# Kernel tuning notes

Measured on AMD Instinct MI355X. Metric: run time of the kernel, lower is better.

Reference implementation:

```python
import jax, jax.numpy as jnp
import numpy as np

N_NODES = 50000
N_EDGES = 800000
N_GRAPHS = 512
F_IN = 128
H = 64


def setup_inputs() -> dict:
    key = jax.random.key(0)
    ks = jax.random.split(key, 12)
    x = jax.random.normal(ks[0], (N_NODES, F_IN), dtype=jnp.float32)
    edge_index = jax.random.randint(ks[1], (2, N_EDGES), 0, N_NODES, dtype=jnp.int64)
    batch = jnp.sort(jax.random.randint(ks[2], (N_NODES,), 0, N_GRAPHS, dtype=jnp.int64))
    def glorot(k, shape):
        lim = float(np.sqrt(6.0 / (shape[0] + shape[1])))
        return jax.random.uniform(k, shape, jnp.float32, -lim, lim)
    return {
        "x": x,
        "edge_index": edge_index,
        "batch": batch,
        "W1": glorot(ks[3], (F_IN, H)), "b1": jnp.zeros((H,), jnp.float32),
        "W2": glorot(ks[4], (H, H)),    "b2": jnp.zeros((H,), jnp.float32),
        "Wf1": glorot(ks[5], (H, 128)), "bf1": jnp.zeros((128,), jnp.float32),
        "Wf2": glorot(ks[6], (128, 1)), "bf2": jnp.zeros((1,), jnp.float32),
    }


def gcn_conv(x, src, dst, norm, W, b):
    # x' = D^{-1/2}(A+I)D^{-1/2} (x W) + b   (self-loops already in src/dst)
    xw = x @ W                                   # [N, H]
    msgs = xw[src] * norm[:, None]               # gather + scale, [E+N, H]
    agg = jax.ops.segment_sum(msgs, dst, num_segments=N_NODES)  # scatter-add
    return agg + b


def reference(x, edge_index, batch, W1, b1, W2, b2, Wf1, bf1, Wf2, bf2):
    loops = jnp.arange(N_NODES, dtype=edge_index.dtype)
    src = jnp.concatenate([edge_index[0], loops])
    dst = jnp.concatenate([edge_index[1], loops])
    # symmetric normalization: deg computed with self-loops, counted at dst
    deg = jax.ops.segment_sum(jnp.ones_like(dst, dtype=x.dtype), dst, num_segments=N_NODES)
    dinv = jax.lax.rsqrt(jnp.maximum(deg, 1.0))
    norm = dinv[src] * dinv[dst]

    h = jax.nn.relu(gcn_conv(x, src, dst, norm, W1, b1))
    h = jax.nn.relu(gcn_conv(h, src, dst, norm, W2, b2))

    # global mean pool over graphs
    sums = jax.ops.segment_sum(h, batch, num_segments=N_GRAPHS)      # [G, H]
    cnts = jax.ops.segment_sum(jnp.ones((N_NODES,), h.dtype), batch, num_segments=N_GRAPHS)
    pooled = sums / jnp.maximum(cnts, 1.0)[:, None]

    out = jax.nn.relu(pooled @ Wf1 + bf1)
    out = out @ Wf2 + bf2
    return out.squeeze(-1)
```

## Files before the change

kernel.cpp:

```cpp
#include <hip/hip_runtime.h>
#include <hip/hip_fp16.h>

#define N_NODES 50000
#define N_EDGES 800000
#define N_GRAPHS 512
#define F_IN 128
#define HDIM 64
#define NBUCK 196
#define BCAP 5120
#define EPB 4096
#define N_P1 ((N_EDGES + EPB - 1) / EPB)
#define MAXPER 20

__global__ __launch_bounds__(256) void pass1_k(const int* __restrict__ src, const int* __restrict__ dst,
                                               int* __restrict__ bucketTot, int* __restrict__ stage) {
    __shared__ int cnt[256];
    __shared__ int goff[256];
    int t = threadIdx.x;
    cnt[t] = 0;
    __syncthreads();
    int base = blockIdx.x * EPB + t * 16;
    int packed[16], meta[16];
    bool full = (blockIdx.x + 1) * EPB <= N_EDGES;
    if (full) {
        const int4* s4 = (const int4*)(src + base);
        const int4* d4 = (const int4*)(dst + base);
        #pragma unroll
        for (int q = 0; q < 4; ++q) {
            int4 sv = s4[q], dv = d4[q];
            int ss[4] = {sv.x, sv.y, sv.z, sv.w};
            int dd[4] = {dv.x, dv.y, dv.z, dv.w};
            #pragma unroll
            for (int j = 0; j < 4; ++j) {
                int b = dd[j] >> 8;
                int r = atomicAdd(&cnt[b], 1);
                packed[q * 4 + j] = ss[j] | ((dd[j] & 255) << 16);
                meta[q * 4 + j] = r | (b << 16);
            }
        }
    } else {
        #pragma unroll
        for (int k = 0; k < 16; ++k) {
            int e = base + k;
            if (e < N_EDGES) {
                int d = dst[e];
                int b = d >> 8;
                int r = atomicAdd(&cnt[b], 1);
                packed[k] = src[e] | ((d & 255) << 16);
                meta[k] = r | (b << 16);
            } else meta[k] = -1;
        }
    }
    __syncthreads();
    if (cnt[t] > 0) goff[t] = atomicAdd(&bucketTot[t], cnt[t]);
    __syncthreads();
    #pragma unroll
    for (int k = 0; k < 16; ++k) {
        if (meta[k] >= 0) {
            int b = meta[k] >> 16, r = meta[k] & 0xFFFF;
            stage[b * BCAP + goff[b] + r] = packed[k];
        }
    }
}

__global__ __launch_bounds__(256) void scanB_k(const int* __restrict__ bucketTot, int* __restrict__ bucketBase,
                                               int* __restrict__ row) {
    __shared__ int s[256];
    int t = threadIdx.x;
    int v = (t < NBUCK) ? bucketTot[t] : 0;
    s[t] = v; __syncthreads();
    for (int off = 1; off < 256; off <<= 1) {
        int u = (t >= off) ? s[t - off] : 0; __syncthreads();
        s[t] += u; __syncthreads();
    }
    if (t < NBUCK) bucketBase[t] = s[t] - v;
    if (t == 0) row[N_NODES] = N_EDGES;
}

__global__ __launch_bounds__(256) void pass2_k(const int* __restrict__ stage, const int* __restrict__ bucketTot,
                                               const int* __restrict__ bucketBase, int* __restrict__ row,
                                               float* __restrict__ dinv, int* __restrict__ csr) {
    __shared__ int cnt[256];
    __shared__ int pf[256];
    __shared__ int lcsr[BCAP];
    int b = blockIdx.x, t = threadIdx.x;
    int tot = bucketTot[b], base = bucketBase[b];
    cnt[t] = 0; __syncthreads();
    int myp[MAXPER], myr[MAXPER];
    #pragma unroll
    for (int k = 0; k < MAXPER; ++k) {
        int i = t + k * 256;
        if (i < tot) {
            int p = stage[b * BCAP + i];
            int loc = (p >> 16) & 255;
            myp[k] = p;
            myr[k] = atomicAdd(&cnt[loc], 1);
        } else myp[k] = -1;
    }
    __syncthreads();
    int cv = cnt[t];
    pf[t] = cv; __syncthreads();
    for (int off = 1; off < 256; off <<= 1) {
        int u = (t >= off) ? pf[t - off] : 0; __syncthreads();
        pf[t] += u; __syncthreads();
    }
    int node = b * 256 + t;
    if (node < N_NODES) {
        row[node] = base + pf[t] - cv;
        dinv[node] = rsqrtf((float)cv + 1.0f);
    }
    #pragma unroll
    for (int k = 0; k < MAXPER; ++k) {
        if (myp[k] >= 0) {
            int loc = (myp[k] >> 16) & 255;
            lcsr[pf[loc] - cnt[loc] + myr[k]] = myp[k] & 0xFFFF;
        }
    }
    __syncthreads();
    for (int i = t; i < tot; i += 256) csr[base + i] = lcsr[i];
}

__global__ __launch_bounds__(256) void xw1_k(const float* __restrict__ x, const float* __restrict__ W1,
                                             const float* __restrict__ dinv, __half* __restrict__ xwh) {
    __shared__ float Ws[F_IN * HDIM];
    __shared__ float xs[64][65];
    int t = threadIdx.x;
    const float4* W4 = (const float4*)W1;
    float4* Ws4 = (float4*)Ws;
    for (int i = t; i < F_IN * HDIM / 4; i += 256) Ws4[i] = W4[i];
    int row0 = blockIdx.x * 64;
    int c4 = t & 15, rg = t >> 4;
    float4 acc[4];
    #pragma unroll
    for (int i = 0; i < 4; ++i) acc[i] = make_float4(0.f, 0.f, 0.f, 0.f);
    const float4* x4 = (const float4*)x;
    for (int kc = 0; kc < 2; ++kc) {
        __syncthreads();
        for (int m = t; m < 1024; m += 256) {
            int n = m >> 4, k4 = m & 15;
            float4 v = make_float4(0.f, 0.f, 0.f, 0.f);
            int gn = row0 + n;
            if (gn < N_NODES) v = x4[gn * 32 + kc * 16 + k4];
            xs[n][k4 * 4 + 0] = v.x; xs[n][k4 * 4 + 1] = v.y;
            xs[n][k4 * 4 + 2] = v.z; xs[n][k4 * 4 + 3] = v.w;
        }
        __syncthreads();
        #pragma unroll 8
        for (int kk = 0; kk < 64; ++kk) {
            float4 wv = Ws4[(kc * 64 + kk) * 16 + c4];
            #pragma unroll
            for (int i = 0; i < 4; ++i) {
                float xv = xs[rg * 4 + i][kk];
                acc[i].x += wv.x * xv; acc[i].y += wv.y * xv;
                acc[i].z += wv.z * xv; acc[i].w += wv.w * xv;
            }
        }
    }
    uint2* xo = (uint2*)xwh;
    #pragma unroll
    for (int i = 0; i < 4; ++i) {
        int n = row0 + rg * 4 + i;
        if (n < N_NODES) {
            float dv = dinv[n];
            __half2 p0 = __float22half2_rn(make_float2(acc[i].x * dv, acc[i].y * dv));
            __half2 p1 = __float22half2_rn(make_float2(acc[i].z * dv, acc[i].w * dv));
            uint2 o;
            o.x = __builtin_bit_cast(unsigned int, p0);
            o.y = __builtin_bit_cast(unsigned int, p1);
            xo[n * 16 + c4] = o;
        }
    }
}

__global__ __launch_bounds__(256) void conv2_k(const float* __restrict__ h1, const float* __restrict__ W2,
                                               const float* __restrict__ dinv, __half* __restrict__ xwh) {
    __shared__ float Ws[HDIM * HDIM];
    __shared__ float hs[64][65];
    int t = threadIdx.x;
    const float4* W4 = (const float4*)W2;
    float4* Ws4 = (float4*)Ws;
    for (int i = t; i < HDIM * HDIM / 4; i += 256) Ws4[i] = W4[i];
    int row0 = blockIdx.x * 64;
    const float4* h4 = (const float4*)h1;
    for (int m = t; m < 1024; m += 256) {
        int n = m >> 4, k4 = m & 15;
        float4 v = make_float4(0.f, 0.f, 0.f, 0.f);
        int gn = row0 + n;
        if (gn < N_NODES) v = h4[gn * 16 + k4];
        hs[n][k4 * 4 + 0] = v.x; hs[n][k4 * 4 + 1] = v.y;
        hs[n][k4 * 4 + 2] = v.z; hs[n][k4 * 4 + 3] = v.w;
    }
    __syncthreads();
    int c4 = t & 15, rg = t >> 4;
    float4 acc[4];
    #pragma unroll
    for (int i = 0; i < 4; ++i) acc[i] = make_float4(0.f, 0.f, 0.f, 0.f);
    #pragma unroll 8
    for (int kk = 0; kk < 64; ++kk) {
        float4 wv = Ws4[kk * 16 + c4];
        #pragma unroll
        for (int i = 0; i < 4; ++i) {
            float xv = hs[rg * 4 + i][kk];
            acc[i].x += wv.x * xv; acc[i].y += wv.y * xv;
            acc[i].z += wv.z * xv; acc[i].w += wv.w * xv;
        }
    }
    uint2* xo = (uint2*)xwh;
    #pragma unroll
    for (int i = 0; i < 4; ++i) {
        int n = row0 + rg * 4 + i;
        if (n < N_NODES) {
            float dv = dinv[n];
            __half2 p0 = __float22half2_rn(make_float2(acc[i].x * dv, acc[i].y * dv));
            __half2 p1 = __float22half2_rn(make_float2(acc[i].z * dv, acc[i].w * dv));
            uint2 o;
            o.x = __builtin_bit_cast(unsigned int, p0);
            o.y = __builtin_bit_cast(unsigned int, p1);
            xo[n * 16 + c4] = o;
        }
    }
}

__device__ inline void acc8(uint4 v, float* a) {
    float2 f;
    f = __half22float2(__builtin_bit_cast(__half2, v.x)); a[0] += f.x; a[1] += f.y;
    f = __half22float2(__builtin_bit_cast(__half2, v.y)); a[2] += f.x; a[3] += f.y;
    f = __half22float2(__builtin_bit_cast(__half2, v.z)); a[4] += f.x; a[5] += f.y;
    f = __half22float2(__builtin_bit_cast(__half2, v.w)); a[6] += f.x; a[7] += f.y;
}

__global__ __launch_bounds__(256) void gather_k(const __half* __restrict__ xwh, const int* __restrict__ row,
                                                const int* __restrict__ csr, const float* __restrict__ dinv,
                                                const float* __restrict__ bias, float* __restrict__ hout) {
    int t = threadIdx.x;
    int node = blockIdx.x * 4 + (t >> 6);
    int lane = t & 63;
    int fq = lane & 7, eslot = lane >> 3;
    const uint4* xw4 = (const uint4*)xwh;
    float a[8];
    #pragma unroll
    for (int k = 0; k < 8; ++k) a[k] = 0.f;
    if (eslot == 0) { uint4 v = xw4[node * 8 + fq]; acc8(v, a); }
    int jend = row[node + 1];
    for (int j = row[node] + eslot; j < jend; j += 8) {
        int s = csr[j];
        uint4 v = xw4[s * 8 + fq];
        acc8(v, a);
    }
    #pragma unroll
    for (int k = 0; k < 8; ++k) {
        a[k] += __shfl_xor(a[k], 8);
        a[k] += __shfl_xor(a[k], 16);
        a[k] += __shfl_xor(a[k], 32);
    }
    if (eslot == 0) {
        float dd = dinv[node];
        const float4* b4 = (const float4*)bias;
        float4 bl = b4[fq * 2], bh = b4[fq * 2 + 1];
        float4 o0, o1;
        o0.x = fmaxf(a[0] * dd + bl.x, 0.f); o0.y = fmaxf(a[1] * dd + bl.y, 0.f);
        o0.z = fmaxf(a[2] * dd + bl.z, 0.f); o0.w = fmaxf(a[3] * dd + bl.w, 0.f);
        o1.x = fmaxf(a[4] * dd + bh.x, 0.f); o1.y = fmaxf(a[5] * dd + bh.y, 0.f);
        o1.z = fmaxf(a[6] * dd + bh.z, 0.f); o1.w = fmaxf(a[7] * dd + bh.w, 0.f);
        float4* ho = (float4*)hout;
        ho[node * 16 + fq * 2] = o0;
        ho[node * 16 + fq * 2 + 1] = o1;
    }
}

__device__ inline int lower_bound_i(const int* __restrict__ a, int n, int v) {
    int lo = 0, hi = n;
    while (lo < hi) { int m = (lo + hi) >> 1; if (a[m] < v) lo = m + 1; else hi = m; }
    return lo;
}

__global__ __launch_bounds__(256) void pool_k(const float* __restrict__ h, const int* __restrict__ batch,
                                              float* __restrict__ pooled) {
    __shared__ int se[2];
    __shared__ float red[4][64];
    int g = blockIdx.x, t = threadIdx.x;
    if (t == 0) { se[0] = lower_bound_i(batch, N_NODES, g); se[1] = lower_bound_i(batch, N_NODES, g + 1); }
    __syncthreads();
    int start = se[0], end = se[1];
    int w = t >> 6, lane = t & 63;
    float acc = 0.f;
    for (int n = start + w; n < end; n += 4) acc += h[n * 64 + lane];
    red[w][lane] = acc; __syncthreads();
    if (w == 0) {
        float v = red[0][lane] + red[1][lane] + red[2][lane] + red[3][lane];
        int c = end - start;
        pooled[g * 64 + lane] = v / (float)max(c, 1);
    }
}

__global__ __launch_bounds__(128) void mlp_k(const float* __restrict__ pooled,
                                             const float* __restrict__ Wf1, const float* __restrict__ bf1,
                                             const float* __restrict__ Wf2, const float* __restrict__ bf2,
                                             float* __restrict__ out) {
    __shared__ float ps[HDIM];
    __shared__ float wsum[2];
    int g = blockIdx.x, t = threadIdx.x;
    if (t < HDIM) ps[t] = pooled[g * HDIM + t];
    __syncthreads();
    float acc = bf1[t];
    #pragma unroll 8
    for (int k = 0; k < HDIM; ++k) acc += ps[k] * Wf1[k * 128 + t];
    acc = fmaxf(acc, 0.f) * Wf2[t];
    #pragma unroll
    for (int off = 32; off > 0; off >>= 1) acc += __shfl_down(acc, off);
    if ((t & 63) == 0) wsum[t >> 6] = acc;
    __syncthreads();
    if (t == 0) out[g] = wsum[0] + wsum[1] + bf2[0];
}

extern "C" void kernel_launch(void* const* d_in, const int* in_sizes, int n_in,
                              void* d_out, int out_size, void* d_ws, size_t ws_size,
                              hipStream_t stream) {
    const float* x    = (const float*)d_in[0];
    const int*   ei   = (const int*)d_in[1];
    const int*   src  = ei;
    const int*   dst  = ei + N_EDGES;
    const int*   batch= (const int*)d_in[2];
    const float* W1   = (const float*)d_in[3];
    const float* b1   = (const float*)d_in[4];
    const float* W2   = (const float*)d_in[5];
    const float* b2   = (const float*)d_in[6];
    const float* Wf1  = (const float*)d_in[7];
    const float* bf1  = (const float*)d_in[8];
    const float* Wf2  = (const float*)d_in[9];
    const float* bf2  = (const float*)d_in[10];
    float* out = (float*)d_out;

    char* p = (char*)d_ws;
    float*  hbuf   = (float*)p;   p += (size_t)N_NODES * HDIM * 4;
    __half* xwh    = (__half*)p;  p += (size_t)N_NODES * HDIM * 2;
    float*  dinv   = (float*)p;   p += (size_t)N_NODES * 4;
    float*  pooled = (float*)p;   p += (size_t)N_GRAPHS * HDIM * 4;
    int*    row    = (int*)p;     p += (size_t)(N_NODES + 1) * 4;
    int*    csr    = (int*)p;     p += (size_t)N_EDGES * 4;
    int*    bTot   = (int*)p;     p += 256 * 4;
    int*    bBase  = (int*)p;     p += 256 * 4;
    int*    stage  = (int*)p;     p += (size_t)NBUCK * BCAP * 4;

    hipMemsetAsync(bTot, 0, 256 * 4, stream);
    pass1_k<<<N_P1, 256, 0, stream>>>(src, dst, bTot, stage);
    scanB_k<<<1, 256, 0, stream>>>(bTot, bBase, row);
    pass2_k<<<NBUCK, 256, 0, stream>>>(stage, bTot, bBase, row, dinv, csr);

    xw1_k<<<(N_NODES + 63) / 64, 256, 0, stream>>>(x, W1, dinv, xwh);
    gather_k<<<N_NODES / 4, 256, 0, stream>>>(xwh, row, csr, dinv, b1, hbuf);
    conv2_k<<<(N_NODES + 63) / 64, 256, 0, stream>>>(hbuf, W2, dinv, xwh);
    gather_k<<<N_NODES / 4, 256, 0, stream>>>(xwh, row, csr, dinv, b2, hbuf);

    pool_k<<<N_GRAPHS, 256, 0, stream>>>(hbuf, batch, pooled);
    mlp_k<<<N_GRAPHS, 128, 0, stream>>>(pooled, Wf1, bf1, Wf2, bf2, out);
}
```

Measured before the change: 224.8 us.

## Coalesce bucket scatter via shared-memory staging and store layer-1 activations in fp16

pass1 now computes a block-local prefix sum over bucket counts, packs edges into shared memory in bucket order, then writes them to global stage buffers contiguously so stores coalesce instead of scattering per thread. Separately, the first gather writes its ReLU output as fp16, which conv2 reads back, halving that intermediate's write and read traffic. The cost is an extra scan plus shared-memory pass in pass1, and some added rounding error in the hidden activations.

Measured after the change: 219.8 us. 1.02x faster.

```diff
diff --git a/kernel.cpp b/kernel.cpp
--- a/kernel.cpp
+++ b/kernel.cpp
@@ -15,12 +15,15 @@
 __global__ __launch_bounds__(256) void pass1_k(const int* __restrict__ src, const int* __restrict__ dst,
                                                int* __restrict__ bucketTot, int* __restrict__ stage) {
     __shared__ int cnt[256];
+    __shared__ int pf[256];
     __shared__ int goff[256];
+    __shared__ int lpk[EPB];
+    __shared__ unsigned char bkn[EPB];
     int t = threadIdx.x;
     cnt[t] = 0;
     __syncthreads();
     int base = blockIdx.x * EPB + t * 16;
-    int packed[16], meta[16];
+    int packed[16], bk[16], rk[16];
     bool full = (blockIdx.x + 1) * EPB <= N_EDGES;
     if (full) {
         const int4* s4 = (const int4*)(src + base);
@@ -33,9 +36,9 @@
             #pragma unroll
             for (int j = 0; j < 4; ++j) {
                 int b = dd[j] >> 8;
-                int r = atomicAdd(&cnt[b], 1);
+                rk[q * 4 + j] = atomicAdd(&cnt[b], 1);
+                bk[q * 4 + j] = b;
                 packed[q * 4 + j] = ss[j] | ((dd[j] & 255) << 16);
-                meta[q * 4 + j] = r | (b << 16);
             }
         }
     } else {
@@ -45,21 +48,35 @@
             if (e < N_EDGES) {
                 int d = dst[e];
                 int b = d >> 8;
-                int r = atomicAdd(&cnt[b], 1);
+                rk[k] = atomicAdd(&cnt[b], 1);
+                bk[k] = b;
                 packed[k] = src[e] | ((d & 255) << 16);
-                meta[k] = r | (b << 16);
-            } else meta[k] = -1;
-        }
-    }
-    __syncthreads();
-    if (cnt[t] > 0) goff[t] = atomicAdd(&bucketTot[t], cnt[t]);
-    __syncthreads();
+            } else bk[k] = -1;
+        }
+    }
+    __syncthreads();
+    int cv = cnt[t];
+    pf[t] = cv; __syncthreads();
+    for (int off = 1; off < 256; off <<= 1) {
+        int u = (t >= off) ? pf[t - off] : 0; __syncthreads();
+        pf[t] += u; __syncthreads();
+    }
+    if (cv > 0) goff[t] = atomicAdd(&bucketTot[t], cv);
     #pragma unroll
     for (int k = 0; k < 16; ++k) {
-        if (meta[k] >= 0) {
-            int b = meta[k] >> 16, r = meta[k] & 0xFFFF;
-            stage[b * BCAP + goff[b] + r] = packed[k];
-        }
+        if (bk[k] >= 0) {
+            int b = bk[k];
+            int p = pf[b] - cnt[b] + rk[k];
+            lpk[p] = packed[k];
+            bkn[p] = (unsigned char)b;
+        }
+    }
+    __syncthreads();
+    int tot = pf[255];
+    for (int i = t; i < tot; i += 256) {
+        int b = bkn[i];
+        int local = i - (pf[b] - cnt[b]);
+        stage[b * BCAP + goff[b] + local] = lpk[i];
     }
 }
 
@@ -172,7 +189,7 @@
     }
 }
 
-__global__ __launch_bounds__(256) void conv2_k(const float* __restrict__ h1, const float* __restrict__ W2,
+__global__ __launch_bounds__(256) void conv2_k(const __half* __restrict__ h1, const float* __restrict__ W2,
                                                const float* __restrict__ dinv, __half* __restrict__ xwh) {
     __shared__ float Ws[HDIM * HDIM];
     __shared__ float hs[64][65];
@@ -181,14 +198,19 @@
     float4* Ws4 = (float4*)Ws;
     for (int i = t; i < HDIM * HDIM / 4; i += 256) Ws4[i] = W4[i];
     int row0 = blockIdx.x * 64;
-    const float4* h4 = (const float4*)h1;
-    for (int m = t; m < 1024; m += 256) {
-        int n = m >> 4, k4 = m & 15;
-        float4 v = make_float4(0.f, 0.f, 0.f, 0.f);
+    const uint4* h8 = (const uint4*)h1;
+    for (int m = t; m < 512; m += 256) {
+        int n = m >> 3, k8 = m & 7;
         int gn = row0 + n;
-        if (gn < N_NODES) v = h4[gn * 16 + k4];
-        hs[n][k4 * 4 + 0] = v.x; hs[n][k4 * 4 + 1] = v.y;
-        hs[n][k4 * 4 + 2] = v.z; hs[n][k4 * 4 + 3] = v.w;
+        uint4 v = make_uint4(0u, 0u, 0u, 0u);
+        if (gn < N_NODES) v = h8[gn * 8 + k8];
+        float2 f0 = __half22float2(__builtin_bit_cast(__half2, v.x));
+        float2 f1 = __half22float2(__builtin_bit_cast(__half2, v.y));
+        float2 f2 = __half22float2(__builtin_bit_cast(__half2, v.z));
+        float2 f3 = __half22float2(__builtin_bit_cast(__half2, v.w));
+        float* hp = &hs[n][k8 * 8];
+        hp[0] = f0.x; hp[1] = f0.y; hp[2] = f1.x; hp[3] = f1.y;
+        hp[4] = f2.x; hp[5] = f2.y; hp[6] = f3.x; hp[7] = f3.y;
     }
     __syncthreads();
     int c4 = t & 15, rg = t >> 4;
@@ -229,9 +251,10 @@
     f = __half22float2(__builtin_bit_cast(__half2, v.w)); a[6] += f.x; a[7] += f.y;
 }
 
+template <bool OUT_HALF>
 __global__ __launch_bounds__(256) void gather_k(const __half* __restrict__ xwh, const int* __restrict__ row,
                                                 const int* __restrict__ csr, const float* __restrict__ dinv,
-                                                const float* __restrict__ bias, float* __restrict__ hout) {
+                                                const float* __restrict__ bias, void* __restrict__ hout) {
     int t = threadIdx.x;
     int node = blockIdx.x * 4 + (t >> 6);
     int lane = t & 63;
@@ -257,14 +280,27 @@
         float dd = dinv[node];
         const float4* b4 = (const float4*)bias;
         float4 bl = b4[fq * 2], bh = b4[fq * 2 + 1];
-        float4 o0, o1;
-        o0.x = fmaxf(a[0] * dd + bl.x, 0.f); o0.y = fmaxf(a[1] * dd + bl.y, 0.f);
-        o0.z = fmaxf(a[2] * dd + bl.z, 0.f); o0.w = fmaxf(a[3] * dd + bl.w, 0.f);
-        o1.x = fmaxf(a[4] * dd + bh.x, 0.f); o1.y = fmaxf(a[5] * dd + bh.y, 0.f);
-        o1.z = fmaxf(a[6] * dd + bh.z, 0.f); o1.w = fmaxf(a[7] * dd + bh.w, 0.f);
-        float4* ho = (float4*)hout;
-        ho[node * 16 + fq * 2] = o0;
-        ho[node * 16 + fq * 2 + 1] = o1;
+        float r[8];
+        r[0] = fmaxf(a[0] * dd + bl.x, 0.f); r[1] = fmaxf(a[1] * dd + bl.y, 0.f);
+        r[2] = fmaxf(a[2] * dd + bl.z, 0.f); r[3] = fmaxf(a[3] * dd + bl.w, 0.f);
+        r[4] = fmaxf(a[4] * dd + bh.x, 0.f); r[5] = fmaxf(a[5] * dd + bh.y, 0.f);
+        r[6] = fmaxf(a[6] * dd + bh.z, 0.f); r[7] = fmaxf(a[7] * dd + bh.w, 0.f);
+        if (OUT_HALF) {
+            __half2 p0 = __float22half2_rn(make_float2(r[0], r[1]));
+            __half2 p1 = __float22half2_rn(make_float2(r[2], r[3]));
+            __half2 p2 = __float22half2_rn(make_float2(r[4], r[5]));
+            __half2 p3 = __float22half2_rn(make_float2(r[6], r[7]));
+            uint4 o;
+            o.x = __builtin_bit_cast(unsigned int, p0);
+            o.y = __builtin_bit_cast(unsigned int, p1);
+            o.z = __builtin_bit_cast(unsigned int, p2);
+            o.w = __builtin_bit_cast(unsigned int, p3);
+            ((uint4*)hout)[node * 8 + fq] = o;
+        } else {
+            float4* ho = (float4*)hout;
+            ho[node * 16 + fq * 2]     = make_float4(r[0], r[1], r[2], r[3]);
+            ho[node * 16 + fq * 2 + 1] = make_float4(r[4], r[5], r[6], r[7]);
+        }
     }
 }
 
@@ -332,7 +368,8 @@
     float* out = (float*)d_out;
 
     char* p = (char*)d_ws;
-    float*  hbuf   = (float*)p;   p += (size_t)N_NODES * HDIM * 4;
+    float*  h2buf  = (float*)p;   p += (size_t)N_NODES * HDIM * 4;
+    __half* h1buf  = (__half*)p;  p += (size_t)N_NODES * HDIM * 2;
     __half* xwh    = (__half*)p;  p += (size_t)N_NODES * HDIM * 2;
     float*  dinv   = (float*)p;   p += (size_t)N_NODES * 4;
     float*  pooled = (float*)p;   p += (size_t)N_GRAPHS * HDIM * 4;
@@ -348,10 +385,10 @@
     pass2_k<<<NBUCK, 256, 0, stream>>>(stage, bTot, bBase, row, dinv, csr);
 
     xw1_k<<<(N_NODES + 63) / 64, 256, 0, stream>>>(x, W1, dinv, xwh);
-    gather_k<<<N_NODES / 4, 256, 0, stream>>>(xwh, row, csr, dinv, b1, hbuf);
-    conv2_k<<<(N_NODES + 63) / 64, 256, 0, stream>>>(hbuf, W2, dinv, xwh);
-    gather_k<<<N_NODES / 4, 256, 0, stream>>>(xwh, row, csr, dinv, b2, hbuf);
-
-    pool_k<<<N_GRAPHS, 256, 0, stream>>>(hbuf, batch, pooled);
+    gather_k<true><<<N_NODES / 4, 256, 0, stream>>>(xwh, row, csr, dinv, b1, (void*)h1buf);
+    conv2_k<<<(N_NODES + 63) / 64, 256, 0, stream>>>(h1buf, W2, dinv, xwh);
+    gather_k<false><<<N_NODES / 4, 256, 0, stream>>>(xwh, row, csr, dinv, b2, (void*)h2buf);
+
+    pool_k<<<N_GRAPHS, 256, 0, stream>>>(h2buf, batch, pooled);
     mlp_k<<<N_GRAPHS, 128, 0, stream>>>(pooled, Wf1, bf1, Wf2, bf2, out);
 }
```
